# Kernel optimization log

Hardware: AMD Instinct MI355X
Metric: run time of the kernel (lower is better)

Reference implementation:

```python
import jax, jax.numpy as jnp
import numpy as np

N, F, E, B, D = 100000, 256, 128, 8192, 32
K = 16  # ceil(D * threshold 0.5): neighbors kept per relation


def setup_inputs() -> dict:
    key = jax.random.key(0)
    ks = jax.random.split(key, 11)
    s = 0.05
    return {
        "features": jax.random.normal(ks[0], (N, F), jnp.float32),
        "nodes": jax.random.randint(ks[1], (B,), 0, N),
        "n1": jax.random.randint(ks[2], (B, D), 0, N),
        "n2": jax.random.randint(ks[3], (B, D), 0, N),
        "n3": jax.random.randint(ks[4], (B, D), 0, N),
        "wc": jax.random.normal(ks[5], (F, 2), jnp.float32) * s,
        "bc": jnp.zeros((2,), jnp.float32),
        "w1": jax.random.normal(ks[6], (F, E), jnp.float32) * s,
        "w2": jax.random.normal(ks[7], (F, E), jnp.float32) * s,
        "w3": jax.random.normal(ks[8], (F, E), jnp.float32) * s,
        "weight": jax.random.normal(ks[9], (3 * E + F, E), jnp.float32) * s,
    }


def reference(features, nodes, n1, n2, n3, wc, bc, w1, w2, w3, weight):
    # label-aware scores for all nodes (label_clf): [N, 2]
    scores = features @ wc + bc
    s1 = scores[:, 1]                      # label-1 logit used for distance
    center_scores = scores[nodes]          # [B, 2]
    c = s1[nodes]                          # [B]

    def relation(neighs, w_r):
        # label-aware filtering: keep K neighbors with scores closest to center
        dist = jnp.abs(s1[neighs] - c[:, None])          # [B, D]
        _, idx = jax.lax.top_k(-dist, K)                 # smallest distances
        sel = jnp.take_along_axis(neighs, idx, axis=1)   # [B, K]
        mean_feats = jnp.mean(features[sel], axis=1)     # [B, F]
        return jax.nn.relu(mean_feats @ w_r)             # [B, E] intra-agg embed

    r1 = relation(n1, w1)
    r2 = relation(n2, w2)
    r3 = relation(n3, w3)

    self_feats = features[nodes]                          # [B, F]
    cat_feats = jnp.concatenate([self_feats, r1, r2, r3], axis=1)  # [B, F+3E]
    combined = jax.nn.relu(cat_feats @ weight).T          # [E, B]
    return combined, center_scores
```

## Files before the change

kernel.cpp:

```cpp
#include <hip/hip_runtime.h>

#define NN 100000
#define FD 256
#define ED 128
#define BB 8192
#define DD 32
#define KSEL 16

typedef unsigned short ushort_t;

static __device__ __forceinline__ float b2f(ushort_t u) {
    union { float f; unsigned int i; } v; v.i = ((unsigned int)u) << 16; return v.f;
}
static __device__ __forceinline__ ushort_t f2b(float f) {
    union { float f; unsigned int i; } v; v.f = f;
    unsigned int x = v.i;
    x += 0x7fffu + ((x >> 16) & 1u);
    return (ushort_t)(x >> 16);
}
static __device__ __forceinline__ int clampid(int v) {
    return v < 0 ? 0 : (v >= NN ? NN - 1 : v);
}


__global__ __launch_bounds__(256) void k_scores(
    const float* __restrict__ feats, const float* __restrict__ wc,
    const float* __restrict__ bc,
    float* __restrict__ s0a, float* __restrict__ s1a)
{
    const int lane = threadIdx.x & 63;
    const int wave = blockIdx.x * 4 + (threadIdx.x >> 6);
    const int nwaves = gridDim.x * 4;

    const float4 wa  = *(const float4*)(wc + lane * 8);
    const float4 wb_ = *(const float4*)(wc + lane * 8 + 4);
    const float w00 = wa.x, w01 = wa.z, w02 = wb_.x, w03 = wb_.z;
    const float w10 = wa.y, w11 = wa.w, w12 = wb_.y, w13 = wb_.w;
    const float bc0 = bc[0], bc1 = bc[1];

    for (int row = wave; row < NN; row += nwaves) {
        const float4 f4 = *(const float4*)(feats + (size_t)row * FD + lane * 4);
        float s0 = f4.x * w00 + f4.y * w01 + f4.z * w02 + f4.w * w03;
        float s1 = f4.x * w10 + f4.y * w11 + f4.z * w12 + f4.w * w13;
        #pragma unroll
        for (int o = 32; o; o >>= 1) {
            s0 += __shfl_xor(s0, o);
            s1 += __shfl_xor(s1, o);
        }
        if (lane == 0) {
            s0a[row] = s0 + bc0;
            s1a[row] = s1 + bc1;
        }
    }
}

__global__ __launch_bounds__(256) void k_rel(
    const float* __restrict__ feats, const float* __restrict__ s1a,
    const int* __restrict__ nodes,
    const int* __restrict__ n1, const int* __restrict__ n2,
    const int* __restrict__ n3,
    const float* __restrict__ w1, const float* __restrict__ w2,
    const float* __restrict__ w3,
    ushort_t* __restrict__ r_buf)
{
    const int r  = blockIdx.y;
    const int b0 = blockIdx.x * 32;
    const int* nr = (r == 0) ? n1 : (r == 1) ? n2 : n3;
    const float* W = (r == 0) ? w1 : (r == 1) ? w2 : w3;

    __shared__ __align__(16) float Am[32][FD];
    __shared__ __align__(16) float Bsm[32 * ED];
    __shared__ int   sl[32 * KSEL];
    __shared__ float cs1[32];
    int* nb = (int*)Bsm;

    const int t    = threadIdx.x;
    const int wv   = t >> 6;
    const int lane = t & 63;

    if (t < 32) cs1[t] = s1a[clampid(nodes[b0 + t])];
    #pragma unroll
    for (int jj = 0; jj < 4; ++jj) {
        const int idx = t + 256 * jj;
        nb[idx] = clampid(nr[(size_t)b0 * DD + idx]);
    }
    __syncthreads();

    #pragma unroll
    for (int jj = 0; jj < 2; ++jj) {
        const int idx = t + 256 * jj;
        sl[idx] = nb[(idx >> 4) * DD + (idx & 15)];
    }
    __syncthreads();

    {
        const int g = t >> 5;
        const int j = t & 31;
        #pragma unroll
        for (int pass = 0; pass < 4; ++pass) {
            const int row = pass * 8 + g;
            const float d = fabsf(s1a[nb[row * DD + j]] - cs1[row]);
            int rank = 0;
            #pragma unroll
            for (int k = 0; k < 32; ++k) {
                const float dk = __shfl(d, k, 32);
                rank += (dk < d) || (dk == d && k < j);
            }
            if (rank < KSEL) sl[row * KSEL + rank] = nb[row * DD + j];
        }
    }
    __syncthreads();

    for (int rr = wv * 8; rr < wv * 8 + 8; ++rr) {
        float a0 = 0.f, a1 = 0.f, a2 = 0.f, a3 = 0.f;
        #pragma unroll
        for (int k = 0; k < KSEL; ++k) {
            const int src = sl[rr * KSEL + k];
            const float4 v = *(const float4*)(feats + (size_t)src * FD + lane * 4);
            a0 += v.x; a1 += v.y; a2 += v.z; a3 += v.w;
        }
        Am[rr][lane * 4 + 0] = a0 * 0.0625f;
        Am[rr][lane * 4 + 1] = a1 * 0.0625f;
        Am[rr][lane * 4 + 2] = a2 * 0.0625f;
        Am[rr][lane * 4 + 3] = a3 * 0.0625f;
    }
    __syncthreads();

    const int bt = (t >> 5) * 4;
    const int et = (t & 31) * 4;
    float acc[4][4] = {};

    for (int k0 = 0; k0 < FD; k0 += 32) {
        #pragma unroll
        for (int jj = 0; jj < 4; ++jj) {
            const int c = t + 256 * jj;
            const int row = c >> 5, col4 = (c & 31) * 4;
            *(float4*)(Bsm + row * ED + col4) =
                *(const float4*)(W + (size_t)(k0 + row) * ED + col4);
        }
        __syncthreads();
        #pragma unroll
        for (int kk = 0; kk < 32; ++kk) {
            const float a0 = Am[bt + 0][k0 + kk];
            const float a1 = Am[bt + 1][k0 + kk];
            const float a2 = Am[bt + 2][k0 + kk];
            const float a3 = Am[bt + 3][k0 + kk];
            const float4 bv = *(const float4*)(Bsm + kk * ED + et);
            acc[0][0] += a0 * bv.x; acc[0][1] += a0 * bv.y;
            acc[0][2] += a0 * bv.z; acc[0][3] += a0 * bv.w;
            acc[1][0] += a1 * bv.x; acc[1][1] += a1 * bv.y;
            acc[1][2] += a1 * bv.z; acc[1][3] += a1 * bv.w;
            acc[2][0] += a2 * bv.x; acc[2][1] += a2 * bv.y;
            acc[2][2] += a2 * bv.z; acc[2][3] += a2 * bv.w;
            acc[3][0] += a3 * bv.x; acc[3][1] += a3 * bv.y;
            acc[3][2] += a3 * bv.z; acc[3][3] += a3 * bv.w;
        }
        __syncthreads();
    }

    #pragma unroll
    for (int i = 0; i < 4; ++i) {
        ushort4 o;
        const float v0 = acc[i][0], v1 = acc[i][1], v2 = acc[i][2], v3 = acc[i][3];
        o.x = f2b(v0 > 0.f ? v0 : 0.f);
        o.y = f2b(v1 > 0.f ? v1 : 0.f);
        o.z = f2b(v2 > 0.f ? v2 : 0.f);
        o.w = f2b(v3 > 0.f ? v3 : 0.f);
        *(ushort4*)(r_buf + (size_t)(r * BB + b0 + bt + i) * ED + et) = o;
    }
}

__global__ __launch_bounds__(256) void k_fin(
    const float* __restrict__ feats, const int* __restrict__ nodes,
    const ushort_t* __restrict__ r_buf, const float* __restrict__ weight,
    const float* __restrict__ s0a, const float* __restrict__ s1a,
    float* __restrict__ out)
{
    const int b0 = blockIdx.x * 32;
    const int e0 = blockIdx.y * 64;
    const int t = threadIdx.x;

    __shared__ __align__(16) unsigned char mem[12800];
    float* Asf = (float*)mem;
    float* Bs2 = (float*)(mem + 4608);
    float* Cs  = (float*)mem;
    __shared__ int nid[32];

    if (t < 32) nid[t] = clampid(nodes[b0 + t]);
    __syncthreads();

    if (blockIdx.y == 0 && t < 64) {
        const int i = t >> 1;
        out[(size_t)ED * BB + (size_t)(b0 + i) * 2 + (t & 1)] =
            (t & 1) ? s1a[nid[i]] : s0a[nid[i]];
    }

    const int arow = t >> 3;
    const int acol = (t & 7) * 4;
    const int bt3 = (t >> 4) * 2;
    const int et3 = (t & 15) * 4;
    float acc[2][4] = {};

    for (int k0 = 0; k0 < FD + 3 * ED; k0 += 32) {
        if (k0 < FD) {
            const float4 v = *(const float4*)(feats + (size_t)nid[arow] * FD + k0 + acol);
            Asf[arow * 36 + acol + 0] = v.x;
            Asf[arow * 36 + acol + 1] = v.y;
            Asf[arow * 36 + acol + 2] = v.z;
            Asf[arow * 36 + acol + 3] = v.w;
        } else {
            const int kr = k0 - FD;
            const ushort4 v = *(const ushort4*)(r_buf +
                (size_t)((kr >> 7) * BB + b0 + arow) * ED + (kr & 127) + acol);
            Asf[arow * 36 + acol + 0] = b2f(v.x);
            Asf[arow * 36 + acol + 1] = b2f(v.y);
            Asf[arow * 36 + acol + 2] = b2f(v.z);
            Asf[arow * 36 + acol + 3] = b2f(v.w);
        }
        #pragma unroll
        for (int jj = 0; jj < 2; ++jj) {
            const int c = t + 256 * jj;
            const int row = c >> 4, col4 = (c & 15) * 4;
            *(float4*)(Bs2 + row * 64 + col4) =
                *(const float4*)(weight + (size_t)(k0 + row) * ED + e0 + col4);
        }
        __syncthreads();
        #pragma unroll
        for (int kk = 0; kk < 32; ++kk) {
            const float a0 = Asf[(bt3 + 0) * 36 + kk];
            const float a1 = Asf[(bt3 + 1) * 36 + kk];
            const float4 bv = *(const float4*)(Bs2 + kk * 64 + et3);
            acc[0][0] += a0 * bv.x; acc[0][1] += a0 * bv.y;
            acc[0][2] += a0 * bv.z; acc[0][3] += a0 * bv.w;
            acc[1][0] += a1 * bv.x; acc[1][1] += a1 * bv.y;
            acc[1][2] += a1 * bv.z; acc[1][3] += a1 * bv.w;
        }
        __syncthreads();
    }

    #pragma unroll
    for (int i = 0; i < 2; ++i)
        #pragma unroll
        for (int j = 0; j < 4; ++j) {
            const float v = acc[i][j];
            Cs[(et3 + j) * 36 + bt3 + i] = v > 0.f ? v : 0.f;
        }
    __syncthreads();
    #pragma unroll
    for (int jj = 0; jj < 2; ++jj) {
        const int c = t + 256 * jj;
        const int er = c >> 3;
        const int off = (c & 7) * 4;
        *(float4*)(out + (size_t)(e0 + er) * BB + b0 + off) =
            *(const float4*)(Cs + er * 36 + off);
    }
}

__global__ __launch_bounds__(256) void k_fused(
    const float* __restrict__ feats, const int* __restrict__ nodes,
    const int* __restrict__ n1, const int* __restrict__ n2,
    const int* __restrict__ n3,
    const float* __restrict__ wc, const float* __restrict__ bc,
    const float* __restrict__ w1, const float* __restrict__ w2,
    const float* __restrict__ w3,
    const float* __restrict__ weight, float* __restrict__ out)
{
    __shared__ __align__(16) unsigned char usm[32768];
    __shared__ int      sl[32 * KSEL];
    __shared__ __align__(16) ushort_t Rt[3 * 32 * ED];
    __shared__ int      nid[32];
    __shared__ float    cs1[32];

    int*      nb  = (int*)usm;
    float*    ns1 = (float*)(usm + 4096);
    ushort_t* Am  = (ushort_t*)usm;
    float*    Bsm = (float*)(usm + 16384);
    float*    Asf = (float*)usm;
    float*    Cs  = (float*)usm;

    const int b0   = blockIdx.x * 32;
    const int t    = threadIdx.x;
    const int wv   = t >> 6;
    const int lane = t & 63;

    const float4 wa  = *(const float4*)(wc + lane * 8);
    const float4 wb_ = *(const float4*)(wc + lane * 8 + 4);
    const float w00 = wa.x, w01 = wa.z, w02 = wb_.x, w03 = wb_.z;
    const float w10 = wa.y, w11 = wa.w, w12 = wb_.y, w13 = wb_.w;
    const float bc0 = bc[0], bc1 = bc[1];

    if (t < 32) nid[t] = clampid(nodes[b0 + t]);
    __syncthreads();

    for (int q = 0; q < 8; ++q) {
        const int i = wv * 8 + q;
        const int node = nid[i];
        const float4 f4 = *(const float4*)(feats + (size_t)node * FD + lane * 4);
        float s0 = f4.x * w00 + f4.y * w01 + f4.z * w02 + f4.w * w03;
        float s1 = f4.x * w10 + f4.y * w11 + f4.z * w12 + f4.w * w13;
        #pragma unroll
        for (int o = 32; o; o >>= 1) {
            s0 += __shfl_xor(s0, o);
            s1 += __shfl_xor(s1, o);
        }
        if (lane == 0) {
            cs1[i] = s1 + bc1;
            out[(size_t)ED * BB + (size_t)(b0 + i) * 2]     = s0 + bc0;
            out[(size_t)ED * BB + (size_t)(b0 + i) * 2 + 1] = s1 + bc1;
        }
    }
    __syncthreads();

    const int bt = (t >> 5) * 4;
    const int et = (t & 31) * 4;

    for (int r = 0; r < 3; ++r) {
        const int* nr = (r == 0) ? n1 : (r == 1) ? n2 : n3;
        const float* W = (r == 0) ? w1 : (r == 1) ? w2 : w3;

        #pragma unroll
        for (int jj = 0; jj < 4; ++jj) {
            const int idx = t + 256 * jj;
            nb[idx] = clampid(nr[(size_t)b0 * DD + idx]);
        }
        __syncthreads();

        #pragma unroll
        for (int jj = 0; jj < 2; ++jj) {
            const int idx = t + 256 * jj;
            sl[idx] = nb[(idx >> 4) * DD + (idx & 15)];
        }

        for (int p = wv; p < 32 * DD; p += 4) {
            const int node = nb[p];
            const float4 f4 = *(const float4*)(feats + (size_t)node * FD + lane * 4);
            float s1 = f4.x * w10 + f4.y * w11 + f4.z * w12 + f4.w * w13;
            #pragma unroll
            for (int o = 32; o; o >>= 1) s1 += __shfl_xor(s1, o);
            if (lane == 0) ns1[p] = s1 + bc1;
        }
        __syncthreads();

        {
            const int g = t >> 5;
            const int j = t & 31;
            #pragma unroll
            for (int pass = 0; pass < 4; ++pass) {
                const int row = pass * 8 + g;
                const float d = fabsf(ns1[row * DD + j] - cs1[row]);
                int rank = 0;
                #pragma unroll
                for (int k = 0; k < 32; ++k) {
                    const float dk = __shfl(d, k, 32);
                    rank += (dk < d) || (dk == d && k < j);
                }
                if (rank < KSEL) sl[row * KSEL + rank] = nb[row * DD + j];
            }
        }
        __syncthreads();

        for (int rr = wv * 8; rr < wv * 8 + 8; ++rr) {
            float a0 = 0.f, a1 = 0.f, a2 = 0.f, a3 = 0.f;
            #pragma unroll
            for (int k = 0; k < KSEL; ++k) {
                const int src = sl[rr * KSEL + k];
                const float4 v = *(const float4*)(feats + (size_t)src * FD + lane * 4);
                a0 += v.x; a1 += v.y; a2 += v.z; a3 += v.w;
            }
            ushort4 o;
            o.x = f2b(a0 * 0.0625f); o.y = f2b(a1 * 0.0625f);
            o.z = f2b(a2 * 0.0625f); o.w = f2b(a3 * 0.0625f);
            *(ushort4*)(Am + rr * FD + lane * 4) = o;
        }
        __syncthreads();

        float acc[4][4] = {};
        for (int k0 = 0; k0 < FD; k0 += 32) {
            #pragma unroll
            for (int jj = 0; jj < 4; ++jj) {
                const int c = t + 256 * jj;
                const int row = c >> 5, col4 = (c & 31) * 4;
                *(float4*)(Bsm + row * ED + col4) =
                    *(const float4*)(W + (size_t)(k0 + row) * ED + col4);
            }
            __syncthreads();
            #pragma unroll
            for (int kk = 0; kk < 32; kk += 4) {
                ushort4 av[4];
                #pragma unroll
                for (int i = 0; i < 4; ++i)
                    av[i] = *(const ushort4*)(Am + (bt + i) * FD + k0 + kk);
                #pragma unroll
                for (int q = 0; q < 4; ++q) {
                    const float4 bv = *(const float4*)(Bsm + (kk + q) * ED + et);
                    const float a0 = b2f(q == 0 ? av[0].x : q == 1 ? av[0].y : q == 2 ? av[0].z : av[0].w);
                    const float a1 = b2f(q == 0 ? av[1].x : q == 1 ? av[1].y : q == 2 ? av[1].z : av[1].w);
                    const float a2 = b2f(q == 0 ? av[2].x : q == 1 ? av[2].y : q == 2 ? av[2].z : av[2].w);
                    const float a3 = b2f(q == 0 ? av[3].x : q == 1 ? av[3].y : q == 2 ? av[3].z : av[3].w);
                    acc[0][0] += a0 * bv.x; acc[0][1] += a0 * bv.y;
                    acc[0][2] += a0 * bv.z; acc[0][3] += a0 * bv.w;
                    acc[1][0] += a1 * bv.x; acc[1][1] += a1 * bv.y;
                    acc[1][2] += a1 * bv.z; acc[1][3] += a1 * bv.w;
                    acc[2][0] += a2 * bv.x; acc[2][1] += a2 * bv.y;
                    acc[2][2] += a2 * bv.z; acc[2][3] += a2 * bv.w;
                    acc[3][0] += a3 * bv.x; acc[3][1] += a3 * bv.y;
                    acc[3][2] += a3 * bv.z; acc[3][3] += a3 * bv.w;
                }
            }
            __syncthreads();
        }

        #pragma unroll
        for (int i = 0; i < 4; ++i) {
            ushort4 o;
            const float v0 = acc[i][0], v1 = acc[i][1], v2 = acc[i][2], v3 = acc[i][3];
            o.x = f2b(v0 > 0.f ? v0 : 0.f);
            o.y = f2b(v1 > 0.f ? v1 : 0.f);
            o.z = f2b(v2 > 0.f ? v2 : 0.f);
            o.w = f2b(v3 > 0.f ? v3 : 0.f);
            *(ushort4*)(Rt + (r * 32 + bt + i) * ED + et) = o;
        }
    }

    const int arow = t >> 3;
    const int acol = (t & 7) * 4;
    float acc[4][4] = {};

    for (int k0 = 0; k0 < FD + 3 * ED; k0 += 32) {
        if (k0 < FD) {
            const float4 v = *(const float4*)(feats + (size_t)nid[arow] * FD + k0 + acol);
            Asf[arow * 36 + acol + 0] = v.x;
            Asf[arow * 36 + acol + 1] = v.y;
            Asf[arow * 36 + acol + 2] = v.z;
            Asf[arow * 36 + acol + 3] = v.w;
        } else {
            const int kr = k0 - FD;
            const ushort4 v = *(const ushort4*)(Rt + ((kr >> 7) * 32 + arow) * ED + (kr & 127) + acol);
            Asf[arow * 36 + acol + 0] = b2f(v.x);
            Asf[arow * 36 + acol + 1] = b2f(v.y);
            Asf[arow * 36 + acol + 2] = b2f(v.z);
            Asf[arow * 36 + acol + 3] = b2f(v.w);
        }
        #pragma unroll
        for (int jj = 0; jj < 4; ++jj) {
            const int c = t + 256 * jj;
            const int row = c >> 5, col4 = (c & 31) * 4;
            *(float4*)(Bsm + row * ED + col4) =
                *(const float4*)(weight + (size_t)(k0 + row) * ED + col4);
        }
        __syncthreads();
        #pragma unroll
        for (int kk = 0; kk < 32; ++kk) {
            const float a0 = Asf[(bt + 0) * 36 + kk];
            const float a1 = Asf[(bt + 1) * 36 + kk];
            const float a2 = Asf[(bt + 2) * 36 + kk];
            const float a3 = Asf[(bt + 3) * 36 + kk];
            const float4 bv = *(const float4*)(Bsm + kk * ED + et);
            acc[0][0] += a0 * bv.x; acc[0][1] += a0 * bv.y;
            acc[0][2] += a0 * bv.z; acc[0][3] += a0 * bv.w;
            acc[1][0] += a1 * bv.x; acc[1][1] += a1 * bv.y;
            acc[1][2] += a1 * bv.z; acc[1][3] += a1 * bv.w;
            acc[2][0] += a2 * bv.x; acc[2][1] += a2 * bv.y;
            acc[2][2] += a2 * bv.z; acc[2][3] += a2 * bv.w;
            acc[3][0] += a3 * bv.x; acc[3][1] += a3 * bv.y;
            acc[3][2] += a3 * bv.z; acc[3][3] += a3 * bv.w;
        }
        __syncthreads();
    }

    #pragma unroll
    for (int i = 0; i < 4; ++i)
        #pragma unroll
        for (int j = 0; j < 4; ++j) {
            const float v = acc[i][j];
            Cs[(et + j) * 36 + bt + i] = v > 0.f ? v : 0.f;
        }
    __syncthreads();
    #pragma unroll
    for (int jj = 0; jj < 4; ++jj) {
        const int c = t + 256 * jj;
        const int er = c >> 3;
        const int off = (c & 7) * 4;
        *(float4*)(out + (size_t)er * BB + b0 + off) = *(const float4*)(Cs + er * 36 + off);
    }
}

extern "C" void kernel_launch(void* const* d_in, const int* in_sizes, int n_in,
                              void* d_out, int out_size, void* d_ws, size_t ws_size,
                              hipStream_t stream)
{
    const float* feats  = (const float*)d_in[0];
    const int*   nodes  = (const int*)d_in[1];
    const int*   n1     = (const int*)d_in[2];
    const int*   n2     = (const int*)d_in[3];
    const int*   n3     = (const int*)d_in[4];
    const float* wc     = (const float*)d_in[5];
    const float* bc     = (const float*)d_in[6];
    const float* w1     = (const float*)d_in[7];
    const float* w2     = (const float*)d_in[8];
    const float* w3     = (const float*)d_in[9];
    const float* weight = (const float*)d_in[10];
    float* out = (float*)d_out;

    if (ws_size >= 7091456) {
        char* ws = (char*)d_ws;
        float*    s0a   = (float*)(ws + 0);
        float*    s1a   = (float*)(ws + 400000);
        ushort_t* r_buf = (ushort_t*)(ws + 800000);

        k_scores<<<800, 256, 0, stream>>>(feats, wc, bc, s0a, s1a);
        k_rel<<<dim3(BB / 32, 3), 256, 0, stream>>>(
            feats, s1a, nodes, n1, n2, n3, w1, w2, w3, r_buf);
        k_fin<<<dim3(BB / 32, 2), 256, 0, stream>>>(
            feats, nodes, r_buf, weight, s0a, s1a, out);
    } else {
        k_fused<<<BB / 32, 256, 0, stream>>>(feats, nodes, n1, n2, n3,
                                             wc, bc, w1, w2, w3, weight, out);
    }
}
```

Before: 298.2 us.

## Store relation mean features as bf16 in LDS and raise k_rel occupancy

The per-block mean-feature tile Am moves from fp32 to bf16, halving its LDS footprint (32 KB to 16 KB) so more blocks can be resident, and launch bounds now request 4 blocks per CU. The gather loop handles two rows per iteration to put more independent global loads in flight, and the inner GEMM reads four bf16 A values per LDS load. Rounding the means to bf16 adds precision loss before the projection and raises conversion ALU work, and the occupancy hint may force register spills.

Result: slower. 313.0 us (+5.0%).

```diff
diff --git a/kernel.cpp b/kernel.cpp
--- a/kernel.cpp
+++ b/kernel.cpp
@@ -54,7 +54,7 @@
     }
 }
 
-__global__ __launch_bounds__(256) void k_rel(
+__global__ __launch_bounds__(256, 4) void k_rel(
     const float* __restrict__ feats, const float* __restrict__ s1a,
     const int* __restrict__ nodes,
     const int* __restrict__ n1, const int* __restrict__ n2,
@@ -68,7 +68,7 @@
     const int* nr = (r == 0) ? n1 : (r == 1) ? n2 : n3;
     const float* W = (r == 0) ? w1 : (r == 1) ? w2 : w3;
 
-    __shared__ __align__(16) float Am[32][FD];
+    __shared__ __align__(16) ushort_t Am[32 * FD];
     __shared__ __align__(16) float Bsm[32 * ED];
     __shared__ int   sl[32 * KSEL];
     __shared__ float cs1[32];
@@ -111,18 +111,25 @@
     }
     __syncthreads();
 
-    for (int rr = wv * 8; rr < wv * 8 + 8; ++rr) {
+    for (int rr = wv * 8; rr < wv * 8 + 8; rr += 2) {
         float a0 = 0.f, a1 = 0.f, a2 = 0.f, a3 = 0.f;
+        float b0v = 0.f, b1v = 0.f, b2v = 0.f, b3v = 0.f;
         #pragma unroll
         for (int k = 0; k < KSEL; ++k) {
-            const int src = sl[rr * KSEL + k];
-            const float4 v = *(const float4*)(feats + (size_t)src * FD + lane * 4);
-            a0 += v.x; a1 += v.y; a2 += v.z; a3 += v.w;
-        }
-        Am[rr][lane * 4 + 0] = a0 * 0.0625f;
-        Am[rr][lane * 4 + 1] = a1 * 0.0625f;
-        Am[rr][lane * 4 + 2] = a2 * 0.0625f;
-        Am[rr][lane * 4 + 3] = a3 * 0.0625f;
+            const int s0i = sl[rr * KSEL + k];
+            const int s1i = sl[(rr + 1) * KSEL + k];
+            const float4 v0 = *(const float4*)(feats + (size_t)s0i * FD + lane * 4);
+            const float4 v1 = *(const float4*)(feats + (size_t)s1i * FD + lane * 4);
+            a0 += v0.x; a1 += v0.y; a2 += v0.z; a3 += v0.w;
+            b0v += v1.x; b1v += v1.y; b2v += v1.z; b3v += v1.w;
+        }
+        ushort4 oa, ob;
+        oa.x = f2b(a0 * 0.0625f);  oa.y = f2b(a1 * 0.0625f);
+        oa.z = f2b(a2 * 0.0625f);  oa.w = f2b(a3 * 0.0625f);
+        ob.x = f2b(b0v * 0.0625f); ob.y = f2b(b1v * 0.0625f);
+        ob.z = f2b(b2v * 0.0625f); ob.w = f2b(b3v * 0.0625f);
+        *(ushort4*)(Am + rr * FD + lane * 4)       = oa;
+        *(ushort4*)(Am + (rr + 1) * FD + lane * 4) = ob;
     }
     __syncthreads();
 
@@ -140,20 +147,27 @@
         }
         __syncthreads();
         #pragma unroll
-        for (int kk = 0; kk < 32; ++kk) {
-            const float a0 = Am[bt + 0][k0 + kk];
-            const float a1 = Am[bt + 1][k0 + kk];
-            const float a2 = Am[bt + 2][k0 + kk];
-            const float a3 = Am[bt + 3][k0 + kk];
-            const float4 bv = *(const float4*)(Bsm + kk * ED + et);
-            acc[0][0] += a0 * bv.x; acc[0][1] += a0 * bv.y;
-            acc[0][2] += a0 * bv.z; acc[0][3] += a0 * bv.w;
-            acc[1][0] += a1 * bv.x; acc[1][1] += a1 * bv.y;
-            acc[1][2] += a1 * bv.z; acc[1][3] += a1 * bv.w;
-            acc[2][0] += a2 * bv.x; acc[2][1] += a2 * bv.y;
-            acc[2][2] += a2 * bv.z; acc[2][3] += a2 * bv.w;
-            acc[3][0] += a3 * bv.x; acc[3][1] += a3 * bv.y;
-            acc[3][2] += a3 * bv.z; acc[3][3] += a3 * bv.w;
+        for (int kk = 0; kk < 32; kk += 4) {
+            ushort4 av[4];
+            #pragma unroll
+            for (int i = 0; i < 4; ++i)
+                av[i] = *(const ushort4*)(Am + (bt + i) * FD + k0 + kk);
+            #pragma unroll
+            for (int q = 0; q < 4; ++q) {
+                const float4 bv = *(const float4*)(Bsm + (kk + q) * ED + et);
+                const float a0 = b2f(q == 0 ? av[0].x : q == 1 ? av[0].y : q == 2 ? av[0].z : av[0].w);
+                const float a1 = b2f(q == 0 ? av[1].x : q == 1 ? av[1].y : q == 2 ? av[1].z : av[1].w);
+                const float a2 = b2f(q == 0 ? av[2].x : q == 1 ? av[2].y : q == 2 ? av[2].z : av[2].w);
+                const float a3 = b2f(q == 0 ? av[3].x : q == 1 ? av[3].y : q == 2 ? av[3].z : av[3].w);
+                acc[0][0] += a0 * bv.x; acc[0][1] += a0 * bv.y;
+                acc[0][2] += a0 * bv.z; acc[0][3] += a0 * bv.w;
+                acc[1][0] += a1 * bv.x; acc[1][1] += a1 * bv.y;
+                acc[1][2] += a1 * bv.z; acc[1][3] += a1 * bv.w;
+                acc[2][0] += a2 * bv.x; acc[2][1] += a2 * bv.y;
+                acc[2][2] += a2 * bv.z; acc[2][3] += a2 * bv.w;
+                acc[3][0] += a3 * bv.x; acc[3][1] += a3 * bv.y;
+                acc[3][2] += a3 * bv.z; acc[3][3] += a3 * bv.w;
+            }
         }
         __syncthreads();
     }
```
